# Performance work log

Hardware: AMD Instinct MI355X
Metric: run time of the kernel (lower is better)

Reference implementation:

```python
import jax, jax.numpy as jnp
import numpy as np

N_NODES = 100000
N_EDGES = 1600000
D = 128
LEAKY_ALPHA = 0.2
ELU_ALPHA = 1.0


def setup_inputs() -> dict:
    key = jax.random.key(0)
    ks = jax.random.split(key, 8)
    s = 0.05
    atom_features = jax.random.normal(ks[0], (N_NODES, D), dtype=jnp.float32)
    W1 = jax.random.normal(ks[1], (1, 2 * D), dtype=jnp.float32) * s
    b1 = jnp.zeros((1,), dtype=jnp.float32)
    W2 = jax.random.normal(ks[2], (D, D), dtype=jnp.float32) * s
    b2 = jnp.zeros((D,), dtype=jnp.float32)
    w_ih = jax.random.normal(ks[3], (3 * D, D), dtype=jnp.float32) * s
    w_hh = jax.random.normal(ks[4], (3 * D, D), dtype=jnp.float32) * s
    b_ih = jnp.zeros((3 * D,), dtype=jnp.float32)
    b_hh = jnp.zeros((3 * D,), dtype=jnp.float32)
    edge_index = jax.random.randint(ks[5], (2, N_EDGES), 0, N_NODES, dtype=jnp.int64)
    return {"atom_features": atom_features, "W1": W1, "b1": b1, "W2": W2,
            "b2": b2, "w_ih": w_ih, "w_hh": w_hh, "b_ih": b_ih, "b_hh": b_hh,
            "edge_index": edge_index}


def _elu(x, alpha):
    return jnp.where(x > 0, x, alpha * (jnp.exp(jnp.minimum(x, 0.0)) - 1.0))


def reference(atom_features, W1, b1, W2, b2, w_ih, w_hh, b_ih, b_hh, edge_index):
    N, d = atom_features.shape
    src = edge_index[0]  # neighbor j (keys[0])
    dst = edge_index[1]  # center node i (keys[1])

    # atom_fc2 transform (dropout is identity in eval)
    nft = atom_features @ W2.T + b2  # [N, d]

    # attention logit per edge: leaky_relu(W1 @ concat(h_dst, h_src) + b1)
    w_d = W1[0, :d]
    w_s = W1[0, d:]
    logit = atom_features @ w_d  # [N]
    logit_src = atom_features @ w_s  # [N]
    score = logit[dst] + logit_src[src] + b1[0]  # [E]
    score = jnp.where(score > 0, score, LEAKY_ALPHA * score)

    # segment softmax over incoming edges of each dst node
    m = jax.ops.segment_max(score, dst, num_segments=N)  # -inf for isolated nodes
    m_safe = jnp.where(jnp.isfinite(m), m, 0.0)
    e = jnp.exp(score - m_safe[dst])  # [E]
    denom = jax.ops.segment_sum(e, dst, num_segments=N)  # [N]
    attn = e / denom[dst]  # [E]

    # weighted scatter-sum of transformed neighbor features
    msg = attn[:, None] * nft[src]  # [E, d]
    transform = jax.ops.segment_sum(msg, dst, num_segments=N)  # [N, d]
    context = _elu(transform, ELU_ALPHA)

    deg = jax.ops.segment_sum(jnp.ones_like(score), dst, num_segments=N)
    out_emb = jnp.where(deg[:, None] > 0, context, atom_features)

    # GRUCell(out_emb, atom_features): torch gate ordering r, z, n
    gi = out_emb @ w_ih.T + b_ih  # [N, 3d]
    gh = atom_features @ w_hh.T + b_hh  # [N, 3d]
    gi_r, gi_z, gi_n = jnp.split(gi, 3, axis=-1)
    gh_r, gh_z, gh_n = jnp.split(gh, 3, axis=-1)
    r = jax.nn.sigmoid(gi_r + gh_r)
    z = jax.nn.sigmoid(gi_z + gh_z)
    n = jnp.tanh(gi_n + r * gh_n)
    h_new = (1.0 - z) * n + z * atom_features
    return h_new
```

## Files before the change

kernel.cpp:

```cpp
#include <hip/hip_runtime.h>
#include <cstdint>
#include <cstddef>

#define D 128
#define LEAKY_ALPHA 0.2f

#define BSHIFT 8
#define BCAP 4608
#define NBUK_MAX 512

typedef __attribute__((ext_vector_type(8))) short short8;
typedef __attribute__((ext_vector_type(4))) short short4v;
typedef __attribute__((ext_vector_type(4))) float f32x4;
typedef __attribute__((ext_vector_type(2))) float f32x2;

static __device__ __forceinline__ unsigned short f32_to_bf16_rne(float v) {
  unsigned x = __float_as_uint(v);
  unsigned r = (x + 0x7fffu + ((x >> 16) & 1u)) >> 16;
  return (unsigned short)r;
}
static __device__ __forceinline__ float bf16_to_f32(unsigned short u) {
  return __uint_as_float(((unsigned)u) << 16);
}

#if __has_builtin(__builtin_amdgcn_cvt_pk_f32_fp8) && __has_builtin(__builtin_amdgcn_cvt_pk_fp8_f32)
#define FP8_HW 1
#endif

static __device__ __forceinline__ unsigned char f32_to_fp8(float x) {
#ifdef FP8_HW
  return (unsigned char)(__builtin_amdgcn_cvt_pk_fp8_f32(x, x, 0, false) & 0xff);
#else
  unsigned u = __float_as_uint(x);
  unsigned s = (u >> 24) & 0x80u;
  unsigned mag = u & 0x7fffffffu;
  if (mag == 0) return (unsigned char)s;
  int e = (int)(mag >> 23) - 127;
  unsigned full = (mag & 0x7fffffu) | 0x800000u;
  if (e >= 9) return (unsigned char)(s | 0x7Eu);
  int sh = (e >= -6) ? 20 : 20 + (-6 - e);
  if (sh > 24) return (unsigned char)s;
  unsigned keep = full >> sh;
  unsigned rem = full & ((1u << sh) - 1u);
  unsigned half = 1u << (sh - 1);
  if (rem > half || (rem == half && (keep & 1u))) keep++;
  unsigned em;
  if (e >= -6) {
    unsigned v = ((unsigned)(e + 7) << 3) + keep - 8u;
    if (v > 0x7Eu) v = 0x7Eu;
    em = v;
  } else {
    em = keep;
  }
  return (unsigned char)(s | em);
#endif
}

#ifndef FP8_HW
static __device__ __forceinline__ float fp8_dec(unsigned b) {
  unsigned em = b & 0x7fu, s = (b & 0x80u) << 24;
  float m;
  if (em >= 8) m = __uint_as_float(0x3C000000u + (em << 20));
  else m = (float)em * 0.001953125f;
  return __uint_as_float(s | __float_as_uint(m));
}
#endif

static __device__ __forceinline__ void fp8_fma16(uint4 u, float e, float* acc) {
#ifdef FP8_HW
  f32x2 t;
  t = __builtin_amdgcn_cvt_pk_f32_fp8(u.x, false); acc[0] += e*t[0]; acc[1] += e*t[1];
  t = __builtin_amdgcn_cvt_pk_f32_fp8(u.x, true ); acc[2] += e*t[0]; acc[3] += e*t[1];
  t = __builtin_amdgcn_cvt_pk_f32_fp8(u.y, false); acc[4] += e*t[0]; acc[5] += e*t[1];
  t = __builtin_amdgcn_cvt_pk_f32_fp8(u.y, true ); acc[6] += e*t[0]; acc[7] += e*t[1];
  t = __builtin_amdgcn_cvt_pk_f32_fp8(u.z, false); acc[8] += e*t[0]; acc[9] += e*t[1];
  t = __builtin_amdgcn_cvt_pk_f32_fp8(u.z, true ); acc[10]+= e*t[0]; acc[11]+= e*t[1];
  t = __builtin_amdgcn_cvt_pk_f32_fp8(u.w, false); acc[12]+= e*t[0]; acc[13]+= e*t[1];
  t = __builtin_amdgcn_cvt_pk_f32_fp8(u.w, true ); acc[14]+= e*t[0]; acc[15]+= e*t[1];
#else
  unsigned ws[4] = {u.x, u.y, u.z, u.w};
  #pragma unroll
  for (int k = 0; k < 4; ++k)
    #pragma unroll
    for (int b = 0; b < 4; ++b)
      acc[k * 4 + b] += e * fp8_dec((ws[k] >> (8 * b)) & 0xffu);
#endif
}

__global__ __launch_bounds__(256) void k_wprep(
    const float* __restrict__ W1, const float* __restrict__ W2,
    const float* __restrict__ w_ih, const float* __restrict__ w_hh,
    unsigned short* __restrict__ Wcat, unsigned short* __restrict__ Wb) {
  int idx = blockIdx.x * 256 + threadIdx.x;
  if (idx < 144 * 128) {
    int r = idx >> 7, c = idx & 127;
    float v = 0.f;
    if (r < 128)      v = W2[r * 128 + c];
    else if (r == 128) v = W1[c];
    else if (r == 129) v = W1[128 + c];
    Wcat[idx] = f32_to_bf16_rne(v);
    return;
  }
  int i2 = idx - 144 * 128;
  if (i2 < 384 * 256) {
    int r = i2 >> 8, c = i2 & 255;
    float v = (c < D) ? w_ih[r * D + c] : w_hh[r * D + (c - D)];
    Wb[i2] = f32_to_bf16_rne(v);
  }
}

#define NPITCH 136
__global__ __launch_bounds__(256, 2) void k_nft_mfma(
    const float* __restrict__ A, const unsigned short* __restrict__ Wcat,
    const float* __restrict__ b2, unsigned char* __restrict__ nftb,
    float* __restrict__ logit_d, float* __restrict__ logit_s,
    unsigned short* __restrict__ X, int N) {
  __shared__ short sA[64 * NPITCH];
  int tid = threadIdx.x;
  int n0 = blockIdx.x * 64;

  #pragma unroll
  for (int i = 0; i < 8; ++i) {
    int g = i * 1024 + tid * 4;
    int row = g >> 7, col = g & 127;
    int gr = n0 + row; if (gr >= N) gr = N - 1;
    float4 v = *(const float4*)&A[(size_t)gr * D + col];
    short4v b;
    b.x = (short)f32_to_bf16_rne(v.x);
    b.y = (short)f32_to_bf16_rne(v.y);
    b.z = (short)f32_to_bf16_rne(v.z);
    b.w = (short)f32_to_bf16_rne(v.w);
    *(short4v*)&sA[row * NPITCH + col] = b;
  }
  __syncthreads();

  int w = tid >> 6, lane = tid & 63, l15 = lane & 15, l4 = lane >> 4;

  f32x4 acc[4][2], acc8[4];
  #pragma unroll
  for (int rt = 0; rt < 4; ++rt) {
    acc[rt][0] = (f32x4)0.f; acc[rt][1] = (f32x4)0.f; acc8[rt] = (f32x4)0.f;
  }

  #pragma unroll
  for (int ks = 0; ks < 4; ++ks) {
    int kk = ks * 32 + l4 * 8;
    short8 a[4];
    #pragma unroll
    for (int rt = 0; rt < 4; ++rt)
      a[rt] = *(const short8*)&sA[(rt * 16 + l15) * NPITCH + kk];
    short8 b0 = *(const short8*)&Wcat[(size_t)(w * 16 + l15) * 128 + kk];
    short8 b1 = *(const short8*)&Wcat[(size_t)((w + 4) * 16 + l15) * 128 + kk];
    #pragma unroll
    for (int rt = 0; rt < 4; ++rt) {
      acc[rt][0] = __builtin_amdgcn_mfma_f32_16x16x32_bf16(a[rt], b0, acc[rt][0], 0, 0, 0);
      acc[rt][1] = __builtin_amdgcn_mfma_f32_16x16x32_bf16(a[rt], b1, acc[rt][1], 0, 0, 0);
    }
    if (w == 0) {
      short8 b2v = *(const short8*)&Wcat[(size_t)(128 + l15) * 128 + kk];
      #pragma unroll
      for (int rt = 0; rt < 4; ++rt)
        acc8[rt] = __builtin_amdgcn_mfma_f32_16x16x32_bf16(a[rt], b2v, acc8[rt], 0, 0, 0);
    }
  }

  #pragma unroll
  for (int i = 0; i < 4; ++i) {
    int g = i * 2048 + tid * 8;
    int row = g >> 7, col = g & 127;
    if (n0 + row < N) {
      short8 v = *(const short8*)&sA[row * NPITCH + col];
      *(short8*)&X[(size_t)(n0 + row) * 256 + 128 + col] = v;
    }
  }

  #pragma unroll
  for (int t = 0; t < 2; ++t) {
    int j = (w + 4 * t) * 16 + l15;
    float bb = b2[j];
    #pragma unroll
    for (int rt = 0; rt < 4; ++rt)
      #pragma unroll
      for (int jr = 0; jr < 4; ++jr) {
        int row = n0 + rt * 16 + l4 * 4 + jr;
        if (row < N)
          nftb[(size_t)row * D + j] = f32_to_fp8(acc[rt][t][jr] + bb);
      }
  }
  if (w == 0 && l15 < 2) {
    float* dst = (l15 == 0) ? logit_d : logit_s;
    #pragma unroll
    for (int rt = 0; rt < 4; ++rt)
      #pragma unroll
      for (int jr = 0; jr < 4; ++jr) {
        int row = n0 + rt * 16 + l4 * 4 + jr;
        if (row < N) dst[row] = acc8[rt][jr];
      }
  }
}

__global__ __launch_bounds__(256) void k_part(
    const int* __restrict__ ei, unsigned* __restrict__ cursors,
    unsigned* __restrict__ part, int E, int NBUK, int EPB) {
  __shared__ int hist[NBUK_MAX];
  __shared__ int sbase[NBUK_MAX];
  int t = threadIdx.x;
  int e0 = blockIdx.x * EPB;
  int e1 = min(e0 + EPB, E);
  for (int i = t; i < NBUK; i += 256) hist[i] = 0;
  __syncthreads();
  for (int e = e0 + t; e < e1; e += 256)
    atomicAdd(&hist[ei[E + e] >> BSHIFT], 1);
  __syncthreads();
  for (int i = t; i < NBUK; i += 256) {
    int h = hist[i];
    sbase[i] = h ? (int)atomicAdd(&cursors[i * 16], (unsigned)h) : 0;
    hist[i] = 0;
  }
  __syncthreads();
  for (int e = e0 + t; e < e1; e += 256) {
    int src = ei[e];
    int dst = ei[E + e];
    int b = dst >> BSHIFT;
    int lp = sbase[b] + atomicAdd(&hist[b], 1);
    if (lp < BCAP)
      part[(size_t)b * BCAP + lp] =
          ((unsigned)(dst & ((1 << BSHIFT) - 1)) << 24) | (unsigned)src;
  }
}

__global__ __launch_bounds__(256) void k_bucket_csr(
    const unsigned* __restrict__ cursors, const unsigned* __restrict__ part,
    const float* __restrict__ logit_s, uint2* __restrict__ rec,
    int2* __restrict__ beg_end, int N) {
  __shared__ unsigned ents[BCAP];
  __shared__ int hist[256];
  __shared__ int scn[256];
  __shared__ int cur[256];
  int b = blockIdx.x, t = threadIdx.x;
  int nb0 = b << BSHIFT;
  int cnt = (int)cursors[b * 16];
  if (cnt > BCAP) cnt = BCAP;
  hist[t] = 0;
  __syncthreads();
  const unsigned* reg = part + (size_t)b * BCAP;
  uint2* rrec = rec + (size_t)b * BCAP;
  for (int i = t; i < cnt; i += 256) {
    unsigned p = reg[i];
    ents[i] = p;
    atomicAdd(&hist[p >> 24], 1);
  }
  __syncthreads();
  int v = hist[t];
  scn[t] = v;
  __syncthreads();
  for (int o = 1; o < 256; o <<= 1) {
    int x = (t >= o) ? scn[t - o] : 0;
    __syncthreads();
    scn[t] += x;
    __syncthreads();
  }
  int excl = scn[t] - v;
  cur[t] = excl;
  int n = nb0 + t;
  if (n < N) beg_end[n] = make_int2(b * BCAP + excl, b * BCAP + excl + v);
  __syncthreads();
  for (int i = t; i < cnt; i += 256) {
    unsigned p = ents[i];
    int lp = atomicAdd(&cur[p >> 24], 1);
    unsigned s = p & 0xFFFFFFu;
    rrec[lp] = make_uint2(s, __float_as_uint(logit_s[s]));
  }
}

#define XPITCH 264
__global__ __launch_bounds__(512, 1) void k_gat_gru(
    const int2* __restrict__ beg_end, const uint2* __restrict__ rec,
    const float* __restrict__ logit_d, const float* __restrict__ b1,
    const unsigned char* __restrict__ nftb,
    const unsigned short* X,
    const unsigned short* __restrict__ Wb,
    const float* __restrict__ b_ih, const float* __restrict__ b_hh,
    float* out, int N) {
  __shared__ short sX[64 * XPITCH];
  int tid = threadIdx.x;
  int n0 = blockIdx.x * 64;

  #pragma unroll
  for (int i = 0; i < 2; ++i) {
    int idx = i * 512 + tid;
    int row = idx >> 4, c8 = idx & 15;
    int gr = n0 + row; if (gr >= N) gr = N - 1;
    short8 v = *(const short8*)&X[(size_t)gr * 256 + 128 + c8 * 8];
    *(short8*)&sX[row * XPITCH + 128 + c8 * 8] = v;
  }
  __syncthreads();

  {
    int l  = tid & 7;
    int nl = tid >> 3;
    int n  = n0 + nl;
    short8 xo0, xo1;
    if (n < N) {
      int2 be = beg_end[n];
      int start = be.x, end = be.y;
      if (end == start) {
        xo0 = *(const short8*)&sX[nl * XPITCH + 128 + l * 16];
        xo1 = *(const short8*)&sX[nl * XPITCH + 128 + l * 16 + 8];
      } else {
        float ld = logit_d[n] + b1[0];
        float acc[16];
        #pragma unroll
        for (int j = 0; j < 16; ++j) acc[j] = 0.f;
        float den = 0.f;
        int p = start;
        for (; p + 4 <= end; p += 4) {
          uint2 r0 = rec[p], r1 = rec[p + 1], r2 = rec[p + 2], r3 = rec[p + 3];
          uint4 u0 = *(const uint4*)&nftb[(size_t)r0.x * D + l * 16];
          uint4 u1 = *(const uint4*)&nftb[(size_t)r1.x * D + l * 16];
          uint4 u2 = *(const uint4*)&nftb[(size_t)r2.x * D + l * 16];
          uint4 u3 = *(const uint4*)&nftb[(size_t)r3.x * D + l * 16];
          float t0 = ld + __uint_as_float(r0.y); t0 = t0 > 0.f ? t0 : LEAKY_ALPHA * t0;
          float t1 = ld + __uint_as_float(r1.y); t1 = t1 > 0.f ? t1 : LEAKY_ALPHA * t1;
          float t2 = ld + __uint_as_float(r2.y); t2 = t2 > 0.f ? t2 : LEAKY_ALPHA * t2;
          float t3 = ld + __uint_as_float(r3.y); t3 = t3 > 0.f ? t3 : LEAKY_ALPHA * t3;
          float e0 = __expf(t0), e1 = __expf(t1), e2 = __expf(t2), e3 = __expf(t3);
          den += (e0 + e1) + (e2 + e3);
          fp8_fma16(u0, e0, acc);
          fp8_fma16(u1, e1, acc);
          fp8_fma16(u2, e2, acc);
          fp8_fma16(u3, e3, acc);
        }
        for (; p < end; ++p) {
          uint2 r = rec[p];
          uint4 u = *(const uint4*)&nftb[(size_t)r.x * D + l * 16];
          float t0 = ld + __uint_as_float(r.y); t0 = t0 > 0.f ? t0 : LEAKY_ALPHA * t0;
          float e0 = __expf(t0);
          den += e0;
          fp8_fma16(u, e0, acc);
        }
        float inv = 1.f / den;
        #pragma unroll
        for (int j = 0; j < 16; ++j) {
          float t = acc[j] * inv;
          float oe = t > 0.f ? t : (__expf(t) - 1.f);
          if (j < 8) xo0[j] = (short)f32_to_bf16_rne(oe);
          else       xo1[j - 8] = (short)f32_to_bf16_rne(oe);
        }
      }
    } else {
      xo0 = (short8)0; xo1 = (short8)0;
    }
    *(short8*)&sX[nl * XPITCH + l * 16]     = xo0;
    *(short8*)&sX[nl * XPITCH + l * 16 + 8] = xo1;
  }
  __syncthreads();

  int w    = tid >> 6;
  int lane = tid & 63;
  int l15  = lane & 15;
  int l4   = lane >> 4;
  int j    = w * 16 + l15;

  f32x4 acc[4][4];
  #pragma unroll
  for (int rt = 0; rt < 4; ++rt)
    #pragma unroll
    for (int q = 0; q < 4; ++q) acc[rt][q] = (f32x4)0.f;

  #pragma unroll
  for (int ks = 0; ks < 8; ++ks) {
    int kk = ks * 32 + l4 * 8;
    short8 a[4];
    #pragma unroll
    for (int rt = 0; rt < 4; ++rt)
      a[rt] = *(const short8*)&sX[(rt * 16 + l15) * XPITCH + kk];
    short8 b0 = *(const short8*)&Wb[(size_t)(j) * 256 + kk];
    short8 b1 = *(const short8*)&Wb[(size_t)(128 + j) * 256 + kk];
    short8 b2 = *(const short8*)&Wb[(size_t)(256 + j) * 256 + kk];
    int qn = (ks < 4) ? 2 : 3;
    #pragma unroll
    for (int rt = 0; rt < 4; ++rt) {
      acc[rt][0]  = __builtin_amdgcn_mfma_f32_16x16x32_bf16(a[rt], b0, acc[rt][0], 0, 0, 0);
      acc[rt][1]  = __builtin_amdgcn_mfma_f32_16x16x32_bf16(a[rt], b1, acc[rt][1], 0, 0, 0);
      acc[rt][qn] = __builtin_amdgcn_mfma_f32_16x16x32_bf16(a[rt], b2, acc[rt][qn], 0, 0, 0);
    }
  }

  float br  = b_ih[j] + b_hh[j];
  float bz  = b_ih[D + j] + b_hh[D + j];
  float bin = b_ih[2 * D + j];
  float bhn = b_hh[2 * D + j];
  #pragma unroll
  for (int rt = 0; rt < 4; ++rt) {
    #pragma unroll
    for (int jr = 0; jr < 4; ++jr) {
      int lrow = rt * 16 + l4 * 4 + jr;
      int row = n0 + lrow;
      if (row < N) {
        float rp  = acc[rt][0][jr] + br;
        float zp  = acc[rt][1][jr] + bz;
        float gin = acc[rt][2][jr] + bin;
        float ghn = acc[rt][3][jr] + bhn;
        float r = 1.f / (1.f + __expf(-rp));
        float z = 1.f / (1.f + __expf(-zp));
        float t = gin + r * ghn;
        float e2 = __expf(2.f * t);
        float nn = 1.f - 2.f / (e2 + 1.f);
        float h = bf16_to_f32((unsigned short)sX[lrow * XPITCH + 128 + j]);
        out[(size_t)row * D + j] = (1.f - z) * nn + z * h;
      }
    }
  }
}

extern "C" void kernel_launch(void* const* d_in, const int* in_sizes, int n_in,
                              void* d_out, int out_size, void* d_ws, size_t ws_size,
                              hipStream_t stream) {
  const float* A    = (const float*)d_in[0];
  const float* W1   = (const float*)d_in[1];
  const float* b1   = (const float*)d_in[2];
  const float* W2   = (const float*)d_in[3];
  const float* b2   = (const float*)d_in[4];
  const float* w_ih = (const float*)d_in[5];
  const float* w_hh = (const float*)d_in[6];
  const float* b_ih = (const float*)d_in[7];
  const float* b_hh = (const float*)d_in[8];
  const int*   ei   = (const int*)d_in[9];

  int N = in_sizes[0] / D;
  int E = in_sizes[9] / 2;
  float* out = (float*)d_out;

  int NBUK = (N + (1 << BSHIFT) - 1) >> BSHIFT;

  char* ws = (char*)d_ws;
  unsigned char* nftb = (unsigned char*)ws;
  float* logit_d = (float*)(ws + (size_t)N * D);
  float* logit_s = logit_d + N;
  int2*  beg_end = (int2*)(logit_s + N);
  unsigned* cursors = (unsigned*)(beg_end + N);
  unsigned* part = cursors + (size_t)NBUK * 16;
  uint2* rec = (uint2*)(part + (size_t)NBUK * BCAP);
  unsigned short* Wb   = (unsigned short*)(rec + (size_t)NBUK * BCAP);
  unsigned short* Wcat = Wb + 384 * 256;

  hipMemsetAsync(cursors, 0, (size_t)NBUK * 16 * sizeof(unsigned), stream);

  k_wprep<<<(144 * 128 + 384 * 256 + 255) / 256, 256, 0, stream>>>(
      W1, W2, w_ih, w_hh, Wcat, Wb);
  k_nft_mfma<<<(N + 63) / 64, 256, 0, stream>>>(A, Wcat, b2, nftb,
                                                logit_d, logit_s,
                                                (unsigned short*)d_out, N);
  int gridPart = 160;
  int EPB = (E + gridPart - 1) / gridPart;
  k_part<<<gridPart, 256, 0, stream>>>(ei, cursors, part, E, NBUK, EPB);
  k_bucket_csr<<<NBUK, 256, 0, stream>>>(cursors, part, logit_s, rec,
                                         beg_end, N);
  k_gat_gru<<<(N + 63) / 64, 512, 0, stream>>>(beg_end, rec, logit_d, b1, nftb,
                                               (const unsigned short*)d_out,
                                               Wb, b_ih, b_hh, out, N);
}
```

Before: 199.3 us.

## Fuse edge partition into feature-transform kernel and precompute edge weights in CSR

Merges the edge bucket-partition kernel into the node-feature MFMA kernel as extra blocks, so the partition runs alongside the GEMM with one fewer launch. The CSR build now computes each edge's leaky-relu score and its exponential once and stores that weight in the record, and the gather loop just reads it. This takes the per-edge exp out of the hot aggregation kernel. The trade-off is extra shared memory in the fused kernel, which may lower occupancy for the GEMM blocks, and no max-subtraction in the softmax, which the old code also skipped.

```diff
diff --git a/kernel.cpp b/kernel.cpp
--- a/kernel.cpp
+++ b/kernel.cpp
@@ -110,13 +110,47 @@
 }
 
 #define NPITCH 136
-__global__ __launch_bounds__(256, 2) void k_nft_mfma(
+__global__ __launch_bounds__(256, 2) void k_front(
     const float* __restrict__ A, const unsigned short* __restrict__ Wcat,
     const float* __restrict__ b2, unsigned char* __restrict__ nftb,
     float* __restrict__ logit_d, float* __restrict__ logit_s,
-    unsigned short* __restrict__ X, int N) {
+    unsigned short* __restrict__ X,
+    const int* __restrict__ ei, unsigned* __restrict__ cursors,
+    unsigned* __restrict__ part,
+    int N, int E, int NBUK, int EPB, int nftBlocks) {
   __shared__ short sA[64 * NPITCH];
+  __shared__ int hist[NBUK_MAX];
+  __shared__ int sbase[NBUK_MAX];
   int tid = threadIdx.x;
+
+  if ((int)blockIdx.x >= nftBlocks) {
+    int t = tid;
+    int pb = blockIdx.x - nftBlocks;
+    int e0 = pb * EPB;
+    int e1 = min(e0 + EPB, E);
+    for (int i = t; i < NBUK; i += 256) hist[i] = 0;
+    __syncthreads();
+    for (int e = e0 + t; e < e1; e += 256)
+      atomicAdd(&hist[ei[E + e] >> BSHIFT], 1);
+    __syncthreads();
+    for (int i = t; i < NBUK; i += 256) {
+      int h = hist[i];
+      sbase[i] = h ? (int)atomicAdd(&cursors[i * 16], (unsigned)h) : 0;
+      hist[i] = 0;
+    }
+    __syncthreads();
+    for (int e = e0 + t; e < e1; e += 256) {
+      int src = ei[e];
+      int dst = ei[E + e];
+      int b = dst >> BSHIFT;
+      int lp = sbase[b] + atomicAdd(&hist[b], 1);
+      if (lp < BCAP)
+        part[(size_t)b * BCAP + lp] =
+            ((unsigned)(dst & ((1 << BSHIFT) - 1)) << 24) | (unsigned)src;
+    }
+    return;
+  }
+
   int n0 = blockIdx.x * 64;
 
   #pragma unroll
@@ -199,49 +233,25 @@
   }
 }
 
-__global__ __launch_bounds__(256) void k_part(
-    const int* __restrict__ ei, unsigned* __restrict__ cursors,
-    unsigned* __restrict__ part, int E, int NBUK, int EPB) {
-  __shared__ int hist[NBUK_MAX];
-  __shared__ int sbase[NBUK_MAX];
-  int t = threadIdx.x;
-  int e0 = blockIdx.x * EPB;
-  int e1 = min(e0 + EPB, E);
-  for (int i = t; i < NBUK; i += 256) hist[i] = 0;
-  __syncthreads();
-  for (int e = e0 + t; e < e1; e += 256)
-    atomicAdd(&hist[ei[E + e] >> BSHIFT], 1);
-  __syncthreads();
-  for (int i = t; i < NBUK; i += 256) {
-    int h = hist[i];
-    sbase[i] = h ? (int)atomicAdd(&cursors[i * 16], (unsigned)h) : 0;
-    hist[i] = 0;
-  }
-  __syncthreads();
-  for (int e = e0 + t; e < e1; e += 256) {
-    int src = ei[e];
-    int dst = ei[E + e];
-    int b = dst >> BSHIFT;
-    int lp = sbase[b] + atomicAdd(&hist[b], 1);
-    if (lp < BCAP)
-      part[(size_t)b * BCAP + lp] =
-          ((unsigned)(dst & ((1 << BSHIFT) - 1)) << 24) | (unsigned)src;
-  }
-}
-
 __global__ __launch_bounds__(256) void k_bucket_csr(
     const unsigned* __restrict__ cursors, const unsigned* __restrict__ part,
-    const float* __restrict__ logit_s, uint2* __restrict__ rec,
+    const float* __restrict__ logit_d, const float* __restrict__ logit_s,
+    const float* __restrict__ b1, uint2* __restrict__ rec,
     int2* __restrict__ beg_end, int N) {
   __shared__ unsigned ents[BCAP];
   __shared__ int hist[256];
   __shared__ int scn[256];
   __shared__ int cur[256];
+  __shared__ float sld[256];
   int b = blockIdx.x, t = threadIdx.x;
   int nb0 = b << BSHIFT;
   int cnt = (int)cursors[b * 16];
   if (cnt > BCAP) cnt = BCAP;
   hist[t] = 0;
+  {
+    int n = nb0 + t;
+    sld[t] = (n < N) ? logit_d[n] + b1[0] : 0.f;
+  }
   __syncthreads();
   const unsigned* reg = part + (size_t)b * BCAP;
   uint2* rrec = rec + (size_t)b * BCAP;
@@ -267,16 +277,18 @@
   __syncthreads();
   for (int i = t; i < cnt; i += 256) {
     unsigned p = ents[i];
-    int lp = atomicAdd(&cur[p >> 24], 1);
+    int dl = p >> 24;
+    int lp = atomicAdd(&cur[dl], 1);
     unsigned s = p & 0xFFFFFFu;
-    rrec[lp] = make_uint2(s, __float_as_uint(logit_s[s]));
+    float sc = sld[dl] + logit_s[s];
+    sc = sc > 0.f ? sc : LEAKY_ALPHA * sc;
+    rrec[lp] = make_uint2(s, __float_as_uint(__expf(sc)));
   }
 }
 
 #define XPITCH 264
 __global__ __launch_bounds__(512, 1) void k_gat_gru(
     const int2* __restrict__ beg_end, const uint2* __restrict__ rec,
-    const float* __restrict__ logit_d, const float* __restrict__ b1,
     const unsigned char* __restrict__ nftb,
     const unsigned short* X,
     const unsigned short* __restrict__ Wb,
@@ -308,7 +320,6 @@
         xo0 = *(const short8*)&sX[nl * XPITCH + 128 + l * 16];
         xo1 = *(const short8*)&sX[nl * XPITCH + 128 + l * 16 + 8];
       } else {
-        float ld = logit_d[n] + b1[0];
         float acc[16];
         #pragma unroll
         for (int j = 0; j < 16; ++j) acc[j] = 0.f;
@@ -320,24 +331,20 @@
           uint4 u1 = *(const uint4*)&nftb[(size_t)r1.x * D + l * 16];
           uint4 u2 = *(const uint4*)&nftb[(size_t)r2.x * D + l * 16];
           uint4 u3 = *(const uint4*)&nftb[(size_t)r3.x * D + l * 16];
-          float t0 = ld + __uint_as_float(r0.y); t0 = t0 > 0.f ? t0 : LEAKY_ALPHA * t0;
-          float t1 = ld + __uint_as_float(r1.y); t1 = t1 > 0.f ? t1 : LEAKY_ALPHA * t1;
-          float t2 = ld + __uint_as_float(r2.y); t2 = t2 > 0.f ? t2 : LEAKY_ALPHA * t2;
-          float t3 = ld + __uint_as_float(r3.y); t3 = t3 > 0.f ? t3 : LEAKY_ALPHA * t3;
-          float e0 = __expf(t0), e1 = __expf(t1), e2 = __expf(t2), e3 = __expf(t3);
-          den += (e0 + e1) + (e2 + e3);
-          fp8_fma16(u0, e0, acc);
-          fp8_fma16(u1, e1, acc);
-          fp8_fma16(u2, e2, acc);
-          fp8_fma16(u3, e3, acc);
+          float w0 = __uint_as_float(r0.y), w1 = __uint_as_float(r1.y);
+          float w2 = __uint_as_float(r2.y), w3 = __uint_as_float(r3.y);
+          den += (w0 + w1) + (w2 + w3);
+          fp8_fma16(u0, w0, acc);
+          fp8_fma16(u1, w1, acc);
+          fp8_fma16(u2, w2, acc);
+          fp8_fma16(u3, w3, acc);
         }
         for (; p < end; ++p) {
           uint2 r = rec[p];
           uint4 u = *(const uint4*)&nftb[(size_t)r.x * D + l * 16];
-          float t0 = ld + __uint_as_float(r.y); t0 = t0 > 0.f ? t0 : LEAKY_ALPHA * t0;
-          float e0 = __expf(t0);
-          den += e0;
-          fp8_fma16(u, e0, acc);
+          float w0 = __uint_as_float(r.y);
+          den += w0;
+          fp8_fma16(u, w0, acc);
         }
         float inv = 1.f / den;
         #pragma unroll
@@ -449,15 +456,17 @@
 
   k_wprep<<<(144 * 128 + 384 * 256 + 255) / 256, 256, 0, stream>>>(
       W1, W2, w_ih, w_hh, Wcat, Wb);
-  k_nft_mfma<<<(N + 63) / 64, 256, 0, stream>>>(A, Wcat, b2, nftb,
-                                                logit_d, logit_s,
-                                                (unsigned short*)d_out, N);
+
+  int nftBlocks = (N + 63) / 64;
   int gridPart = 160;
   int EPB = (E + gridPart - 1) / gridPart;
-  k_part<<<gridPart, 256, 0, stream>>>(ei, cursors, part, E, NBUK, EPB);
-  k_bucket_csr<<<NBUK, 256, 0, stream>>>(cursors, part, logit_s, rec,
-                                         beg_end, N);
-  k_gat_gru<<<(N + 63) / 64, 512, 0, stream>>>(beg_end, rec, logit_d, b1, nftb,
-                                               (const unsigned short*)d_out,
-                                               Wb, b_ih, b_hh, out, N);
-}
+  k_front<<<nftBlocks + gridPart, 256, 0, stream>>>(
+      A, Wcat, b2, nftb, logit_d, logit_s, (unsigned short*)d_out,
+      ei, cursors, part, N, E, NBUK, EPB, nftBlocks);
+
+  k_bucket_csr<<<NBUK, 256, 0, stream>>>(cursors, part, logit_d, logit_s, b1,
+                                         rec, beg_end, N);
+  k_gat_gru<<<nftBlocks, 512, 0, stream>>>(beg_end, rec, nftb,
+                                           (const unsigned short*)d_out,
+                                           Wb, b_ih, b_hh, out, N);
+}
```

Result: faster. 191.8 us (-3.8%).
